# Optimization experiments

Measured on AMD Instinct MI355X. Metric: run time of the kernel, lower is better.

The kernel has to match this reference:

```python
import jax, jax.numpy as jnp
import numpy as np

TOP_K = 2
CAP_FACTOR = 1.25
AUX_COEF = 0.01
Z_COEF = 0.001


def setup_inputs() -> dict:
    key = jax.random.key(0)
    k1, k2 = jax.random.split(key)
    hidden_states = jax.random.normal(k1, (4, 1024, 4096), dtype=jnp.float32)
    # gate_proj weight, torch Linear layout [out=E, in=H]
    W = jax.random.normal(k2, (8, 4096), dtype=jnp.float32) * 0.02
    return {"hidden_states": hidden_states, "W": W}


def reference(hidden_states, W):
    B, S, H = hidden_states.shape
    E = W.shape[0]
    T = B * S
    K = TOP_K
    C = max(int(T * K / E * CAP_FACTOR), 1)  # expert capacity

    x = hidden_states.reshape(T, H)
    gate_logits = x @ W.T                           # [T, E]
    top_v, top_i = jax.lax.top_k(gate_logits, K)    # [T, K]
    top_w = jax.nn.softmax(top_v, axis=-1)          # [T, K]

    # Flatten assignments in (token-major, k-minor) order, matching the
    # sequential python loop. Slot within an expert = number of prior
    # assignments to that expert (exclusive prefix count).
    e = top_i.reshape(-1)                           # [T*K]
    oh = jax.nn.one_hot(e, E, dtype=jnp.int32)      # [T*K, E]
    pos = jnp.sum(jnp.cumsum(oh, axis=0) * oh, axis=-1) - 1  # [T*K]
    valid = pos < C
    pos_c = jnp.minimum(pos, C - 1)
    tok = jnp.arange(T * K) // K
    w = top_w.reshape(-1)

    combine_weights = jnp.zeros((T, E, C), dtype=hidden_states.dtype)
    combine_weights = combine_weights.at[tok, e, pos_c].add(jnp.where(valid, w, 0.0))
    dispatch_mask = jnp.zeros((T, E, C), dtype=jnp.int32)
    dispatch_mask = dispatch_mask.at[tok, e, pos_c].add(valid.astype(jnp.int32)).astype(bool)

    # aux losses (module is in training mode by default)
    gate_probs = jax.nn.softmax(gate_logits, axis=-1)
    mean_gate_prob = gate_probs.mean(axis=0)                      # [E]
    tokens_per_expert = dispatch_mask.sum(axis=(0, 2)).astype(jnp.float32)
    tokens_per_expert = tokens_per_expert / tokens_per_expert.sum()
    load_balancing_loss = AUX_COEF * E * jnp.sum(mean_gate_prob * tokens_per_expert)
    router_z_loss = Z_COEF * jnp.mean(jax.nn.logsumexp(gate_logits, axis=-1))

    return dispatch_mask, combine_weights, top_i, load_balancing_loss, router_z_loss
```

## Files before the change

kernel.cpp:

```cpp
#include <hip/hip_runtime.h>
#include <math.h>

#define TT   4096
#define HH   4096
#define EE   8
#define KTOP 2
#define CAP  1280
#define TEC  ((size_t)TT * EE * CAP)

#define GATE_BLOCKS 256
#define ZERO_BLOCKS 4096
#define ASSIGN_BLOCKS 64

typedef __attribute__((ext_vector_type(4))) float f32x4;


__global__ __launch_bounds__(256) void fused_kernel(
    const float* __restrict__ x, const float* __restrict__ W,
    float* __restrict__ out, float* __restrict__ ws_part,
    int* __restrict__ ws_e, float* __restrict__ ws_w)
{
    int tid = threadIdx.x;

    if (blockIdx.x >= GATE_BLOCKS) {
        size_t zb = blockIdx.x - GATE_BLOCKS;
        f32x4* p = (f32x4*)out;
        const size_t per = (2 * TEC / 4) / ZERO_BLOCKS;
        size_t base = zb * per;
        f32x4 z = {0.f, 0.f, 0.f, 0.f};
#pragma unroll 4
        for (size_t i = tid; i < per; i += 256)
            p[base + i] = z;
        return;
    }

    __shared__ float bacc[9];
    if (tid < 9) bacc[tid] = 0.f;
    __syncthreads();

    int wave = tid >> 6;
    int lane = tid & 63;
    int t0 = (blockIdx.x * 4 + wave) * 4;

    const float4* __restrict__ W4 = (const float4*)W;
    const float4* __restrict__ X4 = (const float4*)x;

    float acc[4][8];
#pragma unroll
    for (int tt = 0; tt < 4; ++tt)
#pragma unroll
        for (int e = 0; e < 8; ++e) acc[tt][e] = 0.f;

    for (int jj = 0; jj < 16; ++jj) {
        int ci = jj * 64 + lane;
        float4 wv[8];
#pragma unroll
        for (int e = 0; e < 8; ++e) wv[e] = W4[e * 1024 + ci];
#pragma unroll
        for (int tt = 0; tt < 4; ++tt) {
            float4 xv = X4[(size_t)(t0 + tt) * 1024 + ci];
#pragma unroll
            for (int e = 0; e < 8; ++e) {
                acc[tt][e] = fmaf(xv.x, wv[e].x, acc[tt][e]);
                acc[tt][e] = fmaf(xv.y, wv[e].y, acc[tt][e]);
                acc[tt][e] = fmaf(xv.z, wv[e].z, acc[tt][e]);
                acc[tt][e] = fmaf(xv.w, wv[e].w, acc[tt][e]);
            }
        }
    }

#pragma unroll
    for (int tt = 0; tt < 4; ++tt)
#pragma unroll
        for (int e = 0; e < 8; ++e) {
#pragma unroll
            for (int s = 32; s >= 1; s >>= 1)
                acc[tt][e] += __shfl_xor(acc[tt][e], s, 64);
        }

    if (lane == 0) {
        for (int tt = 0; tt < 4; ++tt) {
            int t = t0 + tt;
            float l[8];
#pragma unroll
            for (int e = 0; e < 8; ++e) l[e] = acc[tt][e];

            float m = l[0];
#pragma unroll
            for (int e = 1; e < 8; ++e) m = fmaxf(m, l[e]);
            float p[8], s = 0.f;
#pragma unroll
            for (int e = 0; e < 8; ++e) { p[e] = expf(l[e] - m); s += p[e]; }
            float inv = 1.f / s;
#pragma unroll
            for (int e = 0; e < 8; ++e) atomicAdd(&bacc[e], p[e] * inv);
            atomicAdd(&bacc[8], m + logf(s));

            int i0 = 0;
#pragma unroll
            for (int e = 1; e < 8; ++e) if (l[e] > l[i0]) i0 = e;
            int i1 = (i0 == 0) ? 1 : 0;
#pragma unroll
            for (int e = 0; e < 8; ++e) if (e != i0 && l[e] > l[i1]) i1 = e;

            float w0 = 1.f / (1.f + expf(l[i1] - l[i0]));
            float w1 = 1.f - w0;

            float* out_topi = out + 2 * TEC;
            out_topi[t * 2 + 0] = (float)i0;
            out_topi[t * 2 + 1] = (float)i1;
            ws_e[t * 2 + 0] = i0;
            ws_e[t * 2 + 1] = i1;
            ws_w[t * 2 + 0] = w0;
            ws_w[t * 2 + 1] = w1;
        }
    }
    __syncthreads();
    if (tid < 9) ws_part[blockIdx.x * 9 + tid] = bacc[tid];
}

__global__ __launch_bounds__(256) void assign_kernel(
    const int* __restrict__ ws_e, const float* __restrict__ ws_w,
    const float* __restrict__ ws_part, float* __restrict__ out)
{
    __shared__ int   scnt[256][8];
    __shared__ int   ssum[8][8];
    __shared__ int   stot[8];
    __shared__ float lacc[9];

    int tid = threadIdx.x;
    if (tid < 9) lacc[tid] = 0.f;
    __syncthreads();

    if (blockIdx.x == 0) {
#pragma unroll
        for (int j = 0; j < 9; ++j)
            atomicAdd(&lacc[j], ws_part[tid * 9 + j]);
    }

    const int PER = (TT * KTOP) / 256;
    int i0 = tid * PER;
    int cnt[8];
#pragma unroll
    for (int e = 0; e < 8; ++e) cnt[e] = 0;
    for (int j = 0; j < PER; ++j) cnt[ws_e[i0 + j]]++;
#pragma unroll
    for (int e = 0; e < 8; ++e) scnt[tid][e] = cnt[e];
    __syncthreads();

    if (tid < 64) {
        int e = tid & 7, seg = tid >> 3;
        int run = 0;
        for (int j = seg * 32; j < seg * 32 + 32; ++j) {
            int v = scnt[j][e];
            scnt[j][e] = run;
            run += v;
        }
        ssum[seg][e] = run;
    }
    __syncthreads();
    if (tid < 8) {
        int run = 0;
        for (int s = 0; s < 8; ++s) {
            int v = ssum[s][tid];
            ssum[s][tid] = run;
            run += v;
        }
        stot[tid] = run;
    }
    __syncthreads();

    if ((tid >> 2) == blockIdx.x) {
        int seg = tid >> 5;
        int base[8];
#pragma unroll
        for (int e = 0; e < 8; ++e) base[e] = scnt[tid][e] + ssum[seg][e];

        for (int j = 0; j < PER; ++j) {
            int i = i0 + j;
            int e = ws_e[i];
            int pos = base[e]++;
            if (pos < CAP) {
                int tok = i >> 1;
                size_t idx = (size_t)tok * (EE * CAP) + (size_t)e * CAP + pos;
                out[idx] = 1.0f;
                out[TEC + idx] = ws_w[i];
            }
        }
    }

    if (blockIdx.x == 0 && tid == 0) {
        int tot_valid = 0;
        int ve[8];
#pragma unroll
        for (int e = 0; e < 8; ++e) { ve[e] = min(stot[e], CAP); tot_valid += ve[e]; }
        float lbl = 0.f;
#pragma unroll
        for (int e = 0; e < 8; ++e)
            lbl += (lacc[e] / (float)TT) * ((float)ve[e] / (float)tot_valid);
        lbl *= 0.01f * (float)EE;
        float zl = 0.001f * lacc[8] / (float)TT;
        out[2 * TEC + TT * KTOP + 0] = lbl;
        out[2 * TEC + TT * KTOP + 1] = zl;
    }
}

extern "C" void kernel_launch(void* const* d_in, const int* in_sizes, int n_in,
                              void* d_out, int out_size, void* d_ws, size_t ws_size,
                              hipStream_t stream) {
    const float* x = (const float*)d_in[0];
    const float* W = (const float*)d_in[1];
    float* out = (float*)d_out;

    float* ws_part = (float*)d_ws;
    int*   ws_e    = (int*)((char*)d_ws + GATE_BLOCKS * 9 * 4);
    float* ws_w    = (float*)((char*)d_ws + GATE_BLOCKS * 9 * 4 + (size_t)TT * KTOP * 4);

    fused_kernel<<<GATE_BLOCKS + ZERO_BLOCKS, 256, 0, stream>>>(
        x, W, out, ws_part, ws_e, ws_w);

    assign_kernel<<<ASSIGN_BLOCKS, 256, 0, stream>>>(ws_e, ws_w, ws_part, out);
}
```

Before: 111.9 us.

## Interleave gate GEMV and output zeroing in every block, one token per block

Replaces the split grid of 256 gate blocks plus 4096 zeroing blocks with 4096 uniform blocks. Each block computes one token's logits, with the four waves splitting the hidden dimension and combining partials through shared memory, and also zeroes its own slice of the output using nontemporal stores. The aim is to overlap the x read with the large zero-fill write across all CUs instead of serialising them on separate blocks, and to keep the zero stores out of cache. In exchange, the W matrix is re-read by every block rather than reused across four tokens, the per-block partial sums grow to 4096 entries, and the assign kernel now reduces them with a serial loop.

Measured after the change: 92.70 us (median of 2 runs). 17.2% less time.

```diff
diff --git a/kernel.cpp b/kernel.cpp
--- a/kernel.cpp
+++ b/kernel.cpp
@@ -8,8 +8,7 @@
 #define CAP  1280
 #define TEC  ((size_t)TT * EE * CAP)
 
-#define GATE_BLOCKS 256
-#define ZERO_BLOCKS 4096
+#define NBLK 4096
 #define ASSIGN_BLOCKS 64
 
 typedef __attribute__((ext_vector_type(4))) float f32x4;
@@ -20,103 +19,90 @@
     float* __restrict__ out, float* __restrict__ ws_part,
     int* __restrict__ ws_e, float* __restrict__ ws_w)
 {
-    int tid = threadIdx.x;
-
-    if (blockIdx.x >= GATE_BLOCKS) {
-        size_t zb = blockIdx.x - GATE_BLOCKS;
-        f32x4* p = (f32x4*)out;
-        const size_t per = (2 * TEC / 4) / ZERO_BLOCKS;
-        size_t base = zb * per;
+    __shared__ float wpart[4][8];
+
+    int tid  = threadIdx.x;
+    int wave = tid >> 6;
+    int lane = tid & 63;
+    int t    = blockIdx.x;
+
+    const float4* __restrict__ X4 = (const float4*)x + (size_t)t * 1024;
+    const float4* __restrict__ W4 = (const float4*)W;
+
+    float acc[8];
+#pragma unroll
+    for (int e = 0; e < 8; ++e) acc[e] = 0.f;
+
+#pragma unroll
+    for (int j = 0; j < 4; ++j) {
+        int ci = wave * 256 + j * 64 + lane;
+        float4 xv = X4[ci];
+#pragma unroll
+        for (int e = 0; e < 8; ++e) {
+            float4 wv = W4[e * 1024 + ci];
+            acc[e] = fmaf(xv.x, wv.x, acc[e]);
+            acc[e] = fmaf(xv.y, wv.y, acc[e]);
+            acc[e] = fmaf(xv.z, wv.z, acc[e]);
+            acc[e] = fmaf(xv.w, wv.w, acc[e]);
+        }
+    }
+
+#pragma unroll
+    for (int e = 0; e < 8; ++e) {
+#pragma unroll
+        for (int s = 32; s >= 1; s >>= 1)
+            acc[e] += __shfl_xor(acc[e], s, 64);
+    }
+    if (lane == 0) {
+#pragma unroll
+        for (int e = 0; e < 8; ++e) wpart[wave][e] = acc[e];
+    }
+
+    {
+        f32x4* p = (f32x4*)out + (size_t)t * ((2 * TEC / 4) / NBLK);
         f32x4 z = {0.f, 0.f, 0.f, 0.f};
 #pragma unroll 4
-        for (size_t i = tid; i < per; i += 256)
-            p[base + i] = z;
-        return;
-    }
-
-    __shared__ float bacc[9];
-    if (tid < 9) bacc[tid] = 0.f;
-    __syncthreads();
-
-    int wave = tid >> 6;
-    int lane = tid & 63;
-    int t0 = (blockIdx.x * 4 + wave) * 4;
-
-    const float4* __restrict__ W4 = (const float4*)W;
-    const float4* __restrict__ X4 = (const float4*)x;
-
-    float acc[4][8];
-#pragma unroll
-    for (int tt = 0; tt < 4; ++tt)
-#pragma unroll
-        for (int e = 0; e < 8; ++e) acc[tt][e] = 0.f;
-
-    for (int jj = 0; jj < 16; ++jj) {
-        int ci = jj * 64 + lane;
-        float4 wv[8];
-#pragma unroll
-        for (int e = 0; e < 8; ++e) wv[e] = W4[e * 1024 + ci];
-#pragma unroll
-        for (int tt = 0; tt < 4; ++tt) {
-            float4 xv = X4[(size_t)(t0 + tt) * 1024 + ci];
-#pragma unroll
-            for (int e = 0; e < 8; ++e) {
-                acc[tt][e] = fmaf(xv.x, wv[e].x, acc[tt][e]);
-                acc[tt][e] = fmaf(xv.y, wv[e].y, acc[tt][e]);
-                acc[tt][e] = fmaf(xv.z, wv[e].z, acc[tt][e]);
-                acc[tt][e] = fmaf(xv.w, wv[e].w, acc[tt][e]);
-            }
-        }
-    }
-
-#pragma unroll
-    for (int tt = 0; tt < 4; ++tt)
-#pragma unroll
-        for (int e = 0; e < 8; ++e) {
-#pragma unroll
-            for (int s = 32; s >= 1; s >>= 1)
-                acc[tt][e] += __shfl_xor(acc[tt][e], s, 64);
-        }
-
-    if (lane == 0) {
-        for (int tt = 0; tt < 4; ++tt) {
-            int t = t0 + tt;
-            float l[8];
-#pragma unroll
-            for (int e = 0; e < 8; ++e) l[e] = acc[tt][e];
-
-            float m = l[0];
-#pragma unroll
-            for (int e = 1; e < 8; ++e) m = fmaxf(m, l[e]);
-            float p[8], s = 0.f;
-#pragma unroll
-            for (int e = 0; e < 8; ++e) { p[e] = expf(l[e] - m); s += p[e]; }
-            float inv = 1.f / s;
-#pragma unroll
-            for (int e = 0; e < 8; ++e) atomicAdd(&bacc[e], p[e] * inv);
-            atomicAdd(&bacc[8], m + logf(s));
-
-            int i0 = 0;
-#pragma unroll
-            for (int e = 1; e < 8; ++e) if (l[e] > l[i0]) i0 = e;
-            int i1 = (i0 == 0) ? 1 : 0;
-#pragma unroll
-            for (int e = 0; e < 8; ++e) if (e != i0 && l[e] > l[i1]) i1 = e;
-
-            float w0 = 1.f / (1.f + expf(l[i1] - l[i0]));
-            float w1 = 1.f - w0;
-
-            float* out_topi = out + 2 * TEC;
-            out_topi[t * 2 + 0] = (float)i0;
-            out_topi[t * 2 + 1] = (float)i1;
-            ws_e[t * 2 + 0] = i0;
-            ws_e[t * 2 + 1] = i1;
-            ws_w[t * 2 + 0] = w0;
-            ws_w[t * 2 + 1] = w1;
-        }
-    }
-    __syncthreads();
-    if (tid < 9) ws_part[blockIdx.x * 9 + tid] = bacc[tid];
+        for (int i = tid; i < (int)((2 * TEC / 4) / NBLK); i += 256)
+            __builtin_nontemporal_store(z, &p[i]);
+    }
+
+    __syncthreads();
+
+    if (tid == 0) {
+        float l[8];
+#pragma unroll
+        for (int e = 0; e < 8; ++e)
+            l[e] = wpart[0][e] + wpart[1][e] + wpart[2][e] + wpart[3][e];
+
+        float m = l[0];
+#pragma unroll
+        for (int e = 1; e < 8; ++e) m = fmaxf(m, l[e]);
+        float p[8], s = 0.f;
+#pragma unroll
+        for (int e = 0; e < 8; ++e) { p[e] = expf(l[e] - m); s += p[e]; }
+        float inv = 1.f / s;
+#pragma unroll
+        for (int e = 0; e < 8; ++e) ws_part[t * 9 + e] = p[e] * inv;
+        ws_part[t * 9 + 8] = m + logf(s);
+
+        int i0 = 0;
+#pragma unroll
+        for (int e = 1; e < 8; ++e) if (l[e] > l[i0]) i0 = e;
+        int i1 = (i0 == 0) ? 1 : 0;
+#pragma unroll
+        for (int e = 0; e < 8; ++e) if (e != i0 && l[e] > l[i1]) i1 = e;
+
+        float w0 = 1.f / (1.f + expf(l[i1] - l[i0]));
+        float w1 = 1.f - w0;
+
+        float* out_topi = out + 2 * TEC;
+        out_topi[t * 2 + 0] = (float)i0;
+        out_topi[t * 2 + 1] = (float)i1;
+        ws_e[t * 2 + 0] = i0;
+        ws_e[t * 2 + 1] = i1;
+        ws_w[t * 2 + 0] = w0;
+        ws_w[t * 2 + 1] = w1;
+    }
 }
 
 __global__ __launch_bounds__(256) void assign_kernel(
@@ -133,9 +119,16 @@
     __syncthreads();
 
     if (blockIdx.x == 0) {
-#pragma unroll
-        for (int j = 0; j < 9; ++j)
-            atomicAdd(&lacc[j], ws_part[tid * 9 + j]);
+        float r[9];
+#pragma unroll
+        for (int j = 0; j < 9; ++j) r[j] = 0.f;
+        for (int k = 0; k < NBLK / 256; ++k) {
+            const float* q = ws_part + (size_t)(tid * (NBLK / 256) + k) * 9;
+#pragma unroll
+            for (int j = 0; j < 9; ++j) r[j] += q[j];
+        }
+#pragma unroll
+        for (int j = 0; j < 9; ++j) atomicAdd(&lacc[j], r[j]);
     }
 
     const int PER = (TT * KTOP) / 256;
@@ -213,11 +206,10 @@
     float* out = (float*)d_out;
 
     float* ws_part = (float*)d_ws;
-    int*   ws_e    = (int*)((char*)d_ws + GATE_BLOCKS * 9 * 4);
-    float* ws_w    = (float*)((char*)d_ws + GATE_BLOCKS * 9 * 4 + (size_t)TT * KTOP * 4);
-
-    fused_kernel<<<GATE_BLOCKS + ZERO_BLOCKS, 256, 0, stream>>>(
-        x, W, out, ws_part, ws_e, ws_w);
+    int*   ws_e    = (int*)((char*)d_ws + (size_t)NBLK * 9 * 4);
+    float* ws_w    = (float*)((char*)d_ws + (size_t)NBLK * 9 * 4 + (size_t)TT * KTOP * 4);
+
+    fused_kernel<<<NBLK, 256, 0, stream>>>(x, W, out, ws_part, ws_e, ws_w);
 
     assign_kernel<<<ASSIGN_BLOCKS, 256, 0, stream>>>(ws_e, ws_w, ws_part, out);
 }
```
